# Kernel optimization log

Measured on AMD Instinct MI355X. Metric: run time of the kernel, lower is better.

## Reference

```python
import jax, jax.numpy as jnp
import numpy as np
from jax import lax

WBITS = 4
BN_EPS = 1e-5


def quantize_weight_symmetric(w, wbits=WBITS):
    # Per-tensor symmetric uniform quantization with straight-through estimator.
    qmax = float(2 ** (wbits - 1) - 1)  # 7 for 4-bit
    scale = jnp.max(jnp.abs(w)) / qmax
    wq = jnp.clip(jnp.round(w / scale), -qmax, qmax) * scale
    # STE: forward uses wq, backward passes gradient straight through to w
    return w + lax.stop_gradient(wq - w)


def setup_inputs() -> dict:
    key = jax.random.key(0)
    k1, k2 = jax.random.split(key)
    x = jax.random.normal(k1, (32, 128, 56, 56), dtype=jnp.float32)
    w = jax.random.normal(k2, (256, 128, 3, 3), dtype=jnp.float32) * 0.05
    gamma = jnp.ones((256,), dtype=jnp.float32)
    beta = jnp.zeros((256,), dtype=jnp.float32)
    return {"x": x, "w": w, "gamma": gamma, "beta": beta}


def reference(x, w, gamma, beta):
    # Quantized conv (QConv, bias=False, stride=1, padding=1)
    wq = quantize_weight_symmetric(w)
    out = lax.conv_general_dilated(
        x, wq,
        window_strides=(1, 1),
        padding=[(1, 1), (1, 1)],
        dimension_numbers=("NCHW", "OIHW", "NCHW"),
    )  # [N, 256, 56, 56]
    # BatchNorm2d in training mode: batch statistics over (N, H, W)
    mean = jnp.mean(out, axis=(0, 2, 3))
    var = jnp.var(out, axis=(0, 2, 3))
    inv = gamma * lax.rsqrt(var + BN_EPS)
    out = out * inv[None, :, None, None] + (beta - mean * inv)[None, :, None, None]
    # abits=32 -> full-precision activation (ReLU)
    return jax.nn.relu(out)
```

## Files before the change

kernel.cpp:

```cpp
#include <hip/hip_runtime.h>

typedef unsigned short u16;
typedef unsigned int u32;
typedef __attribute__((ext_vector_type(4))) float f32x4;
typedef __attribute__((ext_vector_type(8))) short short8;

#define HWD 56
#define HW2 3136
#define C_IN 128
#define K_OUT 256
#define N_IMG 32
#define CHW_IN 401408
#define CHW_OUT 802816
#define PIX 100352
#define WQ_N 294912
#define XP 58
#define XPP 3364
#define XT_PER_N (XPP*128)
#define NT2 1568

__device__ __forceinline__ u16 f2bf(float f) {
    u32 u = __float_as_uint(f);
    u32 r = u + 0x7FFFu + ((u >> 16) & 1u);
    return (u16)(r >> 16);
}

__device__ __forceinline__ void glds16(const u16* g, u16* l) {
    __builtin_amdgcn_global_load_lds(
        (const __attribute__((address_space(1))) void*)g,
        (__attribute__((address_space(3))) void*)l, 16, 0, 0);
}

__global__ void maxabs_k(const float* __restrict__ w, u32* __restrict__ wsmax) {
    float m = 0.f;
    for (int i = blockIdx.x * blockDim.x + threadIdx.x; i < WQ_N; i += gridDim.x * blockDim.x)
        m = fmaxf(m, fabsf(w[i]));
    for (int off = 32; off; off >>= 1)
        m = fmaxf(m, __shfl_xor(m, off));
    __shared__ float sm[4];
    int lane = threadIdx.x & 63, wid = threadIdx.x >> 6;
    if (lane == 0) sm[wid] = m;
    __syncthreads();
    if (threadIdx.x == 0) {
        float mm = fmaxf(fmaxf(sm[0], sm[1]), fmaxf(sm[2], sm[3]));
        atomicMax(wsmax, __float_as_uint(mm));
    }
}

__global__ void quant_t_k(const float* __restrict__ w, const u32* __restrict__ wsmax,
                          u16* __restrict__ wqt2) {
    int o = blockIdx.x * 256 + threadIdx.x;
    if (o >= WQ_N) return;
    int j = o & 7;
    int t = o >> 3;
    int m = t & 255;
    int t2 = t >> 8;
    int oct8 = t2 & 7;
    int kt = t2 >> 3;
    int c = (kt & 1) * 64 + (oct8 >> 2) * 32 + (oct8 & 3) * 8 + j;
    int tap = kt >> 1;
    float scale = __uint_as_float(wsmax[0]) / 7.0f;
    float q = rintf(w[(m * 128 + c) * 9 + tap] / scale);
    q = fminf(fmaxf(q, -7.0f), 7.0f);
    wqt2[o] = f2bf(q * scale);
}

__global__ void halo_zero(u16* __restrict__ xt) {
    int i = blockIdx.x * 256 + threadIdx.x;
    if (i >= 32 * 3648) return;
    int n = i / 3648, t = i - n * 3648;
    int site = t >> 4, chunk = t & 15;
    int h, w;
    if (site < 58)       { h = 0;          w = site; }
    else if (site < 116) { h = 57;         w = site - 58; }
    else if (site < 172) { h = site - 115; w = 0; }
    else                 { h = site - 171; w = 57; }
    *(uint4*)(xt + ((size_t)n * XPP + h * XP + w) * 128 + chunk * 8) = (uint4){0, 0, 0, 0};
}

__global__ __launch_bounds__(256) void pad_transpose(const float* __restrict__ x,
                                                     u16* __restrict__ xt) {
    __shared__ float T[128][57];
    const int tid = threadIdx.x;
    const int n = blockIdx.x / HWD;
    const int h = blockIdx.x - n * HWD;
    const float* src = x + (size_t)n * CHW_IN + h * HWD;
    #pragma unroll
    for (int it = 0; it < 7; ++it) {
        int i = tid + it * 256;
        int c = i / 14, q = i - c * 14;
        float4 v = *(const float4*)(src + c * HW2 + q * 4);
        T[c][q * 4 + 0] = v.x; T[c][q * 4 + 1] = v.y;
        T[c][q * 4 + 2] = v.z; T[c][q * 4 + 3] = v.w;
    }
    __syncthreads();
    u16* dst = xt + ((size_t)n * XPP + (h + 1) * XP + 1) * 128;
    #pragma unroll
    for (int it = 0; it < 4; ++it) {
        int i = tid + it * 256;
        if (i < 56 * 16) {
            int w = i >> 4, oc = i & 15;
            union { u16 us[8]; uint4 v4; } pk;
            #pragma unroll
            for (int j = 0; j < 8; ++j) pk.us[j] = f2bf(T[oc * 8 + j][w]);
            *(uint4*)(dst + (size_t)w * 128 + oc * 8) = pk.v4;
        }
    }
}

__global__ __launch_bounds__(512, 2) void conv8(const u16* __restrict__ xt,
                                                const u16* __restrict__ wqt2,
                                                float* __restrict__ out,
                                                float* __restrict__ P) {
    __shared__ __align__(16) u16 lds[2][4][8192];
    const int tid = threadIdx.x;
    const int lane = tid & 63;
    const int w8 = tid >> 6;
    const int wm = w8 >> 2, wn = w8 & 3;
    const int fr = lane & 15, fq = lane >> 4;
    const int nt = (blockIdx.x & 7) * 49 + (blockIdx.x >> 3);
    const int pixbase = nt * 256;

    const int octB = w8 >> 1;
    const int pg0 = (w8 & 1) * 2;
    u32 site[2];
    #pragma unroll
    for (int r = 0; r < 2; ++r) {
        int p = pixbase + (pg0 + r) * 64 + lane;
        int n = p / HW2; int hw = p - n * HW2;
        int h = hw / HWD; int ww = hw - h * HWD;
        site[r] = (u32)(n * XT_PER_N + (h * XP + ww) * 128);
    }

#define STAGE_A(bf, S, kh) do {                                                  \
        const u16* g_ = wqt2 + (S) * 16384 + (kh) * 8192 + (w8 * 2) * 512 + lane * 8; \
        glds16(g_,       &lds[bf][kh][(w8 * 2 + 0) * 512]);                      \
        glds16(g_ + 512, &lds[bf][kh][(w8 * 2 + 1) * 512]);                      \
    } while (0)
#define STAGE_B(bf, S, kh) do {                                                  \
        int tap_ = (S) >> 1, ch_ = (S) & 1;                                      \
        int r_ = tap_ / 3, s_ = tap_ - r_ * 3;                                   \
        u32 off_ = (u32)((r_ * XP + s_) * 128 + ch_ * 64 + (kh) * 32 + octB * 8);\
        glds16(xt + site[0] + off_, &lds[bf][2 + (kh)][(octB * 4 + pg0 + 0) * 512]); \
        glds16(xt + site[1] + off_, &lds[bf][2 + (kh)][(octB * 4 + pg0 + 1) * 512]); \
    } while (0)
#define LOAD_A(dst, bf, kh, h_)                                                   \
        _Pragma("unroll") for (int mi = 0; mi < 4; ++mi)                          \
            dst[mi] = *(const short8*)&lds[bf][kh][fq * 2048 + ((size_t)(wm * 128 + (h_) * 64 + mi * 16 + fr)) * 8];
#define LOAD_B(dst, bf, kh)                                                       \
        _Pragma("unroll") for (int ni = 0; ni < 4; ++ni)                          \
            dst[ni] = *(const short8*)&lds[bf][2 + (kh)][fq * 2048 + ((size_t)(wn * 64 + ni * 16 + fr)) * 8];
#define MMA(h_, af_, bf_) do {                                                    \
        __builtin_amdgcn_s_setprio(1);                                            \
        _Pragma("unroll") for (int mi = 0; mi < 4; ++mi)                          \
            _Pragma("unroll") for (int ni = 0; ni < 4; ++ni)                      \
                acc[(h_) * 4 + mi][ni] = __builtin_amdgcn_mfma_f32_16x16x32_bf16( \
                    af_[mi], bf_[ni], acc[(h_) * 4 + mi][ni], 0, 0, 0);           \
        __builtin_amdgcn_s_setprio(0);                                            \
    } while (0)
#define BAR() __builtin_amdgcn_s_barrier()
#define WLG0() asm volatile("s_waitcnt lgkmcnt(0)" ::: "memory")

    f32x4 acc[8][4];
    #pragma unroll
    for (int a = 0; a < 8; ++a)
        #pragma unroll
        for (int b = 0; b < 4; ++b)
            acc[a][b] = (f32x4){0.f, 0.f, 0.f, 0.f};

    STAGE_A(0, 0, 0); STAGE_A(0, 0, 1); STAGE_B(0, 0, 0); STAGE_B(0, 0, 1);
    STAGE_B(1, 1, 0); STAGE_A(1, 1, 0); STAGE_B(1, 1, 1);
    asm volatile("s_waitcnt vmcnt(6)" ::: "memory");
    BAR();

    #pragma unroll 1
    for (int i = 0; i < 9; ++i) {
        const int t2 = 2 * i + 2, t3 = 2 * i + 3;
        const bool st = (i < 8);
        short8 a0[4], a1[4], b0[4], b1[4];
        LOAD_A(a0, 0, 0, 0); LOAD_B(b0, 0, 0);
        STAGE_A(1, 2 * i + 1, 1);
        BAR(); WLG0(); MMA(0, a0, b0); BAR();
        LOAD_A(a1, 0, 0, 1);
        if (st) STAGE_B(0, t2, 0);
        BAR(); WLG0(); MMA(1, a1, b0); BAR();
        LOAD_A(a0, 0, 1, 0); LOAD_B(b1, 0, 1);
        if (st) STAGE_A(0, t2, 0);
        BAR(); WLG0(); MMA(0, a0, b1); BAR();
        if (i == 8) asm volatile("s_waitcnt vmcnt(0)" ::: "memory");
        else        asm volatile("s_waitcnt vmcnt(4)" ::: "memory");
        LOAD_A(a1, 0, 1, 1);
        if (st) STAGE_B(0, t2, 1);
        BAR(); WLG0(); MMA(1, a1, b1); BAR();
        LOAD_A(a0, 1, 0, 0); LOAD_B(b0, 1, 0);
        if (st) STAGE_A(0, t2, 1);
        BAR(); WLG0(); MMA(0, a0, b0); BAR();
        LOAD_A(a1, 1, 0, 1);
        if (st) STAGE_B(1, t3, 0);
        BAR(); WLG0(); MMA(1, a1, b0); BAR();
        LOAD_A(a0, 1, 1, 0); LOAD_B(b1, 1, 1);
        if (st) STAGE_A(1, t3, 0);
        BAR(); WLG0(); MMA(0, a0, b1); BAR();
        if (i == 8) asm volatile("s_waitcnt vmcnt(0)" ::: "memory");
        else        asm volatile("s_waitcnt vmcnt(4)" ::: "memory");
        LOAD_A(a1, 1, 1, 1);
        if (st) STAGE_B(1, t3, 1);
        BAR(); WLG0(); MMA(1, a1, b1); BAR();
    }
#undef STAGE_A
#undef STAGE_B
#undef LOAD_A
#undef LOAD_B
#undef MMA
#undef BAR
#undef WLG0

    #pragma unroll
    for (int ni = 0; ni < 4; ++ni) {
        int pix = pixbase + wn * 64 + ni * 16 + fr;
        int n = pix / HW2;
        int hw = pix - n * HW2;
        int obase = n * CHW_OUT + hw;
        #pragma unroll
        for (int h = 0; h < 2; ++h)
            #pragma unroll
            for (int mi = 0; mi < 4; ++mi) {
                int ch = wm * 128 + h * 64 + mi * 16 + fq * 4;
                #pragma unroll
                for (int j = 0; j < 4; ++j)
                    out[obase + (ch + j) * HW2] = acc[h * 4 + mi][ni][j];
            }
    }

    #pragma unroll
    for (int h = 0; h < 2; ++h)
        #pragma unroll
        for (int mi = 0; mi < 4; ++mi)
            #pragma unroll
            for (int j = 0; j < 4; ++j) {
                float s = 0.f, q = 0.f;
                #pragma unroll
                for (int ni = 0; ni < 4; ++ni) {
                    float v = acc[h * 4 + mi][ni][j];
                    s += v; q += v * v;
                }
                #pragma unroll
                for (int msk = 1; msk < 16; msk <<= 1) {
                    s += __shfl_xor(s, msk);
                    q += __shfl_xor(q, msk);
                }
                if (fr == 0) {
                    int ch = wm * 128 + h * 64 + mi * 16 + fq * 4 + j;
                    float* dst = P + ((size_t)(nt * 4 + wn) * 256 + ch) * 2;
                    dst[0] = s; dst[1] = q;
                }
            }
}

__global__ void stats_fin(const float* __restrict__ P, const float* __restrict__ gamma,
                          const float* __restrict__ beta, float* __restrict__ stats) {
    int ch = blockIdx.x;
    int tid = threadIdx.x;
    float s = 0.f, q = 0.f;
    for (int i = tid; i < NT2; i += 256) {
        const float* p = P + ((size_t)i * 256 + ch) * 2;
        s += p[0]; q += p[1];
    }
    for (int m = 32; m; m >>= 1) { s += __shfl_xor(s, m); q += __shfl_xor(q, m); }
    __shared__ float ss[4], qs[4];
    int l = tid & 63, w = tid >> 6;
    if (l == 0) { ss[w] = s; qs[w] = q; }
    __syncthreads();
    if (tid == 0) {
        float S = ss[0] + ss[1] + ss[2] + ss[3];
        float Q = qs[0] + qs[1] + qs[2] + qs[3];
        float mean = S / (float)PIX;
        float var = Q / (float)PIX - mean * mean;
        float inv = gamma[ch] * rsqrtf(var + 1e-5f);
        stats[2 * ch] = inv;
        stats[2 * ch + 1] = beta[ch] - mean * inv;
    }
}

__global__ void bn_relu_k(float* __restrict__ out, const float* __restrict__ stats) {
    const int n4 = (N_IMG * CHW_OUT) / 4;
    int stride = gridDim.x * blockDim.x;
    for (int i = blockIdx.x * blockDim.x + threadIdx.x; i < n4; i += stride) {
        int ch = (i / (HW2 / 4)) & (K_OUT - 1);
        float inv = stats[2 * ch], sh = stats[2 * ch + 1];
        f32x4 v = ((f32x4*)out)[i];
        #pragma unroll
        for (int j = 0; j < 4; ++j)
            v[j] = fmaxf(v[j] * inv + sh, 0.f);
        ((f32x4*)out)[i] = v;
    }
}

extern "C" void kernel_launch(void* const* d_in, const int* in_sizes, int n_in,
                              void* d_out, int out_size, void* d_ws, size_t ws_size,
                              hipStream_t stream) {
    const float* x = (const float*)d_in[0];
    const float* w = (const float*)d_in[1];
    const float* gamma = (const float*)d_in[2];
    const float* beta = (const float*)d_in[3];
    float* out = (float*)d_out;

    char* ws = (char*)d_ws;
    u32* wsmax = (u32*)ws;
    float* stats = (float*)(ws + 64);
    u16* wqt2 = (u16*)(ws + 4096);
    u16* xt = (u16*)(ws + (1u << 20));
    float* P = (float*)(ws + 29360128u);

    hipMemsetAsync(wsmax, 0, 64, stream);
    maxabs_k<<<128, 256, 0, stream>>>(w, wsmax);
    quant_t_k<<<WQ_N / 256, 256, 0, stream>>>(w, wsmax, wqt2);
    halo_zero<<<456, 256, 0, stream>>>(xt);
    pad_transpose<<<N_IMG * HWD, 256, 0, stream>>>(x, xt);
    conv8<<<392, 512, 0, stream>>>(xt, wqt2, out, P);
    stats_fin<<<K_OUT, 256, 0, stream>>>(P, gamma, beta, stats);
    bn_relu_k<<<4096, 256, 0, stream>>>(out, stats);
}
```

Before: 161.1 us.

## Software-pipeline LDS fragment loads, store conv output as bf16, transpose partial stats

The conv main loop now loads the next A/B fragments from LDS before issuing the current MFMA block, with scheduling barriers. This removes one barrier per step and lets LDS reads overlap the matrix math. When the workspace is large enough, the conv writes its pre-BN result as bf16 to scratch instead of fp32 into the output. The BN/ReLU kernel then reads half the bytes, at the cost of rounding the pre-normalization values to bf16. Partial statistics are stored channel-major so the finalize kernel reads them contiguously with float2 loads.

```diff
diff --git a/kernel.cpp b/kernel.cpp
--- a/kernel.cpp
+++ b/kernel.cpp
@@ -18,6 +18,8 @@
 #define XPP 3364
 #define XT_PER_N (XPP*128)
 #define NT2 1568
+#define CV_OFF 33554432u
+#define WS_NEED_BF16 (CV_OFF + (size_t)PIX * K_OUT * 2)
 
 __device__ __forceinline__ u16 f2bf(float f) {
     u32 u = __float_as_uint(f);
@@ -108,9 +110,11 @@
     }
 }
 
+template <bool BF16OUT>
 __global__ __launch_bounds__(512, 2) void conv8(const u16* __restrict__ xt,
                                                 const u16* __restrict__ wqt2,
                                                 float* __restrict__ out,
+                                                u16* __restrict__ cvout,
                                                 float* __restrict__ P) {
     __shared__ __align__(16) u16 lds[2][4][8192];
     const int tid = threadIdx.x;
@@ -160,6 +164,8 @@
     } while (0)
 #define BAR() __builtin_amdgcn_s_barrier()
 #define WLG0() asm volatile("s_waitcnt lgkmcnt(0)" ::: "memory")
+#define SCHED0() __builtin_amdgcn_sched_barrier(0)
+#define GATE(n_) asm volatile("s_waitcnt vmcnt(" #n_ ")" ::: "memory")
 
     f32x4 acc[8][4];
     #pragma unroll
@@ -168,44 +174,47 @@
         for (int b = 0; b < 4; ++b)
             acc[a][b] = (f32x4){0.f, 0.f, 0.f, 0.f};
 
+    short8 ra[4], rna[4], rb[4], rnb[4];
+
     STAGE_A(0, 0, 0); STAGE_A(0, 0, 1); STAGE_B(0, 0, 0); STAGE_B(0, 0, 1);
     STAGE_B(1, 1, 0); STAGE_A(1, 1, 0); STAGE_B(1, 1, 1);
-    asm volatile("s_waitcnt vmcnt(6)" ::: "memory");
+    GATE(6);
     BAR();
+    LOAD_A(ra, 0, 0, 0); LOAD_B(rb, 0, 0);
+    WLG0(); SCHED0();
 
     #pragma unroll 1
     for (int i = 0; i < 9; ++i) {
         const int t2 = 2 * i + 2, t3 = 2 * i + 3;
         const bool st = (i < 8);
-        short8 a0[4], a1[4], b0[4], b1[4];
-        LOAD_A(a0, 0, 0, 0); LOAD_B(b0, 0, 0);
         STAGE_A(1, 2 * i + 1, 1);
-        BAR(); WLG0(); MMA(0, a0, b0); BAR();
-        LOAD_A(a1, 0, 0, 1);
+        LOAD_A(rna, 0, 0, 1);
+        SCHED0(); MMA(0, ra, rb); WLG0(); SCHED0(); BAR();
         if (st) STAGE_B(0, t2, 0);
-        BAR(); WLG0(); MMA(1, a1, b0); BAR();
-        LOAD_A(a0, 0, 1, 0); LOAD_B(b1, 0, 1);
+        LOAD_A(ra, 0, 1, 0); LOAD_B(rnb, 0, 1);
+        SCHED0(); MMA(1, rna, rb); WLG0(); SCHED0(); BAR();
         if (st) STAGE_A(0, t2, 0);
-        BAR(); WLG0(); MMA(0, a0, b1); BAR();
-        if (i == 8) asm volatile("s_waitcnt vmcnt(0)" ::: "memory");
-        else        asm volatile("s_waitcnt vmcnt(4)" ::: "memory");
-        LOAD_A(a1, 0, 1, 1);
+        LOAD_A(rna, 0, 1, 1);
+        SCHED0(); MMA(0, ra, rnb); WLG0(); SCHED0(); BAR();
+        if (i == 8) GATE(0); else GATE(4);
         if (st) STAGE_B(0, t2, 1);
-        BAR(); WLG0(); MMA(1, a1, b1); BAR();
-        LOAD_A(a0, 1, 0, 0); LOAD_B(b0, 1, 0);
+        LOAD_A(ra, 1, 0, 0); LOAD_B(rb, 1, 0);
+        SCHED0(); MMA(1, rna, rnb); WLG0(); SCHED0(); BAR();
         if (st) STAGE_A(0, t2, 1);
-        BAR(); WLG0(); MMA(0, a0, b0); BAR();
-        LOAD_A(a1, 1, 0, 1);
+        LOAD_A(rna, 1, 0, 1);
+        SCHED0(); MMA(0, ra, rb); WLG0(); SCHED0(); BAR();
         if (st) STAGE_B(1, t3, 0);
-        BAR(); WLG0(); MMA(1, a1, b0); BAR();
-        LOAD_A(a0, 1, 1, 0); LOAD_B(b1, 1, 1);
+        LOAD_A(ra, 1, 1, 0); LOAD_B(rnb, 1, 1);
+        SCHED0(); MMA(1, rna, rb); WLG0(); SCHED0(); BAR();
         if (st) STAGE_A(1, t3, 0);
-        BAR(); WLG0(); MMA(0, a0, b1); BAR();
-        if (i == 8) asm volatile("s_waitcnt vmcnt(0)" ::: "memory");
-        else        asm volatile("s_waitcnt vmcnt(4)" ::: "memory");
-        LOAD_A(a1, 1, 1, 1);
-        if (st) STAGE_B(1, t3, 1);
-        BAR(); WLG0(); MMA(1, a1, b1); BAR();
+        LOAD_A(rna, 1, 1, 1);
+        SCHED0(); MMA(0, ra, rnb); WLG0(); SCHED0(); BAR();
+        if (i == 8) GATE(0); else GATE(4);
+        if (st) {
+            STAGE_B(1, t3, 1);
+            LOAD_A(ra, 0, 0, 0); LOAD_B(rb, 0, 0);
+        }
+        SCHED0(); MMA(1, rna, rnb); WLG0(); SCHED0(); BAR();
     }
 #undef STAGE_A
 #undef STAGE_B
@@ -214,24 +223,31 @@
 #undef MMA
 #undef BAR
 #undef WLG0
+#undef SCHED0
+#undef GATE
 
     #pragma unroll
     for (int ni = 0; ni < 4; ++ni) {
         int pix = pixbase + wn * 64 + ni * 16 + fr;
         int n = pix / HW2;
         int hw = pix - n * HW2;
-        int obase = n * CHW_OUT + hw;
+        size_t obase = (size_t)n * CHW_OUT + hw;
         #pragma unroll
         for (int h = 0; h < 2; ++h)
             #pragma unroll
             for (int mi = 0; mi < 4; ++mi) {
                 int ch = wm * 128 + h * 64 + mi * 16 + fq * 4;
                 #pragma unroll
-                for (int j = 0; j < 4; ++j)
-                    out[obase + (ch + j) * HW2] = acc[h * 4 + mi][ni][j];
+                for (int j = 0; j < 4; ++j) {
+                    if (BF16OUT)
+                        cvout[obase + (size_t)(ch + j) * HW2] = f2bf(acc[h * 4 + mi][ni][j]);
+                    else
+                        out[obase + (size_t)(ch + j) * HW2] = acc[h * 4 + mi][ni][j];
+                }
             }
     }
 
+    const int slice = nt * 4 + wn;
     #pragma unroll
     for (int h = 0; h < 2; ++h)
         #pragma unroll
@@ -251,7 +267,7 @@
                 }
                 if (fr == 0) {
                     int ch = wm * 128 + h * 64 + mi * 16 + fq * 4 + j;
-                    float* dst = P + ((size_t)(nt * 4 + wn) * 256 + ch) * 2;
+                    float* dst = P + ((size_t)ch * NT2 + slice) * 2;
                     dst[0] = s; dst[1] = q;
                 }
             }
@@ -262,9 +278,10 @@
     int ch = blockIdx.x;
     int tid = threadIdx.x;
     float s = 0.f, q = 0.f;
+    const float* base = P + (size_t)ch * NT2 * 2;
     for (int i = tid; i < NT2; i += 256) {
-        const float* p = P + ((size_t)i * 256 + ch) * 2;
-        s += p[0]; q += p[1];
+        float2 v = *(const float2*)(base + i * 2);
+        s += v.x; q += v.y;
     }
     for (int m = 32; m; m >>= 1) { s += __shfl_xor(s, m); q += __shfl_xor(q, m); }
     __shared__ float ss[4], qs[4];
@@ -282,7 +299,7 @@
     }
 }
 
-__global__ void bn_relu_k(float* __restrict__ out, const float* __restrict__ stats) {
+__global__ void bn_relu_f32(float* __restrict__ out, const float* __restrict__ stats) {
     const int n4 = (N_IMG * CHW_OUT) / 4;
     int stride = gridDim.x * blockDim.x;
     for (int i = blockIdx.x * blockDim.x + threadIdx.x; i < n4; i += stride) {
@@ -293,6 +310,27 @@
         for (int j = 0; j < 4; ++j)
             v[j] = fmaxf(v[j] * inv + sh, 0.f);
         ((f32x4*)out)[i] = v;
+    }
+}
+
+__global__ void bn_relu_bf16(const u16* __restrict__ cvout, float* __restrict__ out,
+                             const float* __restrict__ stats) {
+    const int n8 = (N_IMG * CHW_OUT) / 8;
+    int stride = gridDim.x * blockDim.x;
+    for (int i = blockIdx.x * blockDim.x + threadIdx.x; i < n8; i += stride) {
+        int ch = (i / (HW2 / 8)) & (K_OUT - 1);
+        float inv = stats[2 * ch], sh = stats[2 * ch + 1];
+        short8 v = ((const short8*)cvout)[i];
+        f32x4 o0, o1;
+        #pragma unroll
+        for (int j = 0; j < 4; ++j) {
+            float a = __uint_as_float(((u32)(u16)v[j]) << 16);
+            float b = __uint_as_float(((u32)(u16)v[j + 4]) << 16);
+            o0[j] = fmaxf(a * inv + sh, 0.f);
+            o1[j] = fmaxf(b * inv + sh, 0.f);
+        }
+        ((f32x4*)out)[i * 2] = o0;
+        ((f32x4*)out)[i * 2 + 1] = o1;
     }
 }
 
@@ -311,13 +349,21 @@
     u16* wqt2 = (u16*)(ws + 4096);
     u16* xt = (u16*)(ws + (1u << 20));
     float* P = (float*)(ws + 29360128u);
+    u16* cvout = (u16*)(ws + CV_OFF);
+    const bool bf16path = (ws_size >= WS_NEED_BF16);
 
     hipMemsetAsync(wsmax, 0, 64, stream);
     maxabs_k<<<128, 256, 0, stream>>>(w, wsmax);
     quant_t_k<<<WQ_N / 256, 256, 0, stream>>>(w, wsmax, wqt2);
     halo_zero<<<456, 256, 0, stream>>>(xt);
     pad_transpose<<<N_IMG * HWD, 256, 0, stream>>>(x, xt);
-    conv8<<<392, 512, 0, stream>>>(xt, wqt2, out, P);
-    stats_fin<<<K_OUT, 256, 0, stream>>>(P, gamma, beta, stats);
-    bn_relu_k<<<4096, 256, 0, stream>>>(out, stats);
-}
+    if (bf16path) {
+        conv8<true><<<392, 512, 0, stream>>>(xt, wqt2, out, cvout, P);
+        stats_fin<<<K_OUT, 256, 0, stream>>>(P, gamma, beta, stats);
+        bn_relu_bf16<<<4096, 256, 0, stream>>>(cvout, out, stats);
+    } else {
+        conv8<false><<<392, 512, 0, stream>>>(xt, wqt2, out, cvout, P);
+        stats_fin<<<K_OUT, 256, 0, stream>>>(P, gamma, beta, stats);
+        bn_relu_f32<<<4096, 256, 0, stream>>>(out, stats);
+    }
+}
```

New measurement: 147.5 us. 8.4% less time.
